# Optimization experiments

Measured on AMD Instinct MI355X. Metric: run time of the kernel, lower is better.

The kernel has to match this reference:

```python
import jax, jax.numpy as jnp
import numpy as np

H, DK = 16, 64
D = H * DK  # d_model = 1024
B, S = 2, 2048


def setup_inputs() -> dict:
    key = jax.random.key(0)
    ks = jax.random.split(key, 11)
    std = 1.0 / np.sqrt(D)
    inp = {
        "query": jax.random.normal(ks[0], (B, S, D), dtype=jnp.float32),
        "key": jax.random.normal(ks[1], (B, S, D), dtype=jnp.float32),
        "value": jax.random.normal(ks[2], (B, S, D), dtype=jnp.float32),
        "Wq": jax.random.normal(ks[3], (D, D), dtype=jnp.float32) * std,
        "bq": jnp.zeros((D,), dtype=jnp.float32),
        "Wk": jax.random.normal(ks[4], (D, D), dtype=jnp.float32) * std,
        "bk": jnp.zeros((D,), dtype=jnp.float32),
        "Wv": jax.random.normal(ks[5], (D, D), dtype=jnp.float32) * std,
        "bv": jnp.zeros((D,), dtype=jnp.float32),
        "Wo": jax.random.normal(ks[6], (D, D), dtype=jnp.float32) * std,
        "bo": jnp.zeros((D,), dtype=jnp.float32),
    }
    return inp


def reference(query, key, value, Wq, bq, Wk, bk, Wv, bv, Wo, bo):
    # torch.nn.Linear convention: y = x @ W.T + b
    def split_heads(x):
        b, s, _ = x.shape
        return x.reshape(b, s, H, DK).transpose(0, 2, 1, 3)  # [B,H,S,DK]

    q = split_heads(query @ Wq.T + bq)
    k = split_heads(key @ Wk.T + bk)
    v = split_heads(value @ Wv.T + bv)

    scale = 1.0 / jnp.sqrt(jnp.asarray(DK, dtype=q.dtype))
    scores = jnp.einsum("bhqd,bhkd->bhqk", q, k) * scale  # [B,H,S,S]
    p_attn = jax.nn.softmax(scores, axis=-1)
    ctx = jnp.einsum("bhqk,bhkd->bhqd", p_attn, v)  # [B,H,S,DK]

    ctx = ctx.transpose(0, 2, 1, 3).reshape(query.shape[0], -1, H * DK)
    return ctx @ Wo.T + bo
```

## Files before the change

### kernel.cpp

```cpp
#include <hip/hip_runtime.h>
#include <stdint.h>

#define BATCH 2
#define SEQ   2048
#define NHEAD 16
#define DK    64
#define DMODEL 1024
#define MROWS (BATCH*SEQ)

typedef __attribute__((ext_vector_type(8))) __bf16 bf16x8;
typedef __attribute__((ext_vector_type(4))) float f32x4;
typedef __attribute__((ext_vector_type(8))) unsigned short u16x8;
typedef __attribute__((ext_vector_type(4))) unsigned short u16x4;
typedef __attribute__((ext_vector_type(4))) unsigned int u32x4;

#define QSCALE 0.18033688f

__device__ __forceinline__ unsigned short f2bf(float f) {
  union { float f; uint32_t u; } c; c.f = f;
  uint32_t u = c.u;
  return (unsigned short)((u + 0x7fffu + ((u >> 16) & 1u)) >> 16);
}

__device__ __forceinline__ void gld16(const void* g, void* lds) {
  __builtin_amdgcn_global_load_lds(
      (const __attribute__((address_space(1))) void*)g,
      (__attribute__((address_space(3))) void*)lds,
      16, 0, 0);
}

__global__ __launch_bounds__(256)
void cvt_all(const float* __restrict__ q, const float* __restrict__ k, const float* __restrict__ v,
             const float* __restrict__ Wq, const float* __restrict__ Wk,
             const float* __restrict__ Wv, const float* __restrict__ Wo,
             unsigned short* __restrict__ Xq, unsigned short* __restrict__ Xk,
             unsigned short* __restrict__ Xv,
             unsigned short* __restrict__ Wqb, unsigned short* __restrict__ Wkb,
             unsigned short* __restrict__ Wvb, unsigned short* __restrict__ Wob) {
  int blk = blockIdx.x;
  const float* in; unsigned short* out; int base;
  if (blk < 6144) {
    int ti = blk >> 11;
    in  = (ti == 0) ? q  : (ti == 1) ? k  : v;
    out = (ti == 0) ? Xq : (ti == 1) ? Xk : Xv;
    base = (blk & 2047) * 2048;
  } else {
    int ti = (blk - 6144) >> 9;
    in  = (ti == 0) ? Wq  : (ti == 1) ? Wk  : (ti == 2) ? Wv  : Wo;
    out = (ti == 0) ? Wqb : (ti == 1) ? Wkb : (ti == 2) ? Wvb : Wob;
    base = ((blk - 6144) & 511) * 2048;
  }
  int i = base + threadIdx.x * 8;
  float4 a = *(const float4*)(in + i);
  float4 b = *(const float4*)(in + i + 4);
  u16x8 o;
  o[0]=f2bf(a.x); o[1]=f2bf(a.y); o[2]=f2bf(a.z); o[3]=f2bf(a.w);
  o[4]=f2bf(b.x); o[5]=f2bf(b.y); o[6]=f2bf(b.z); o[7]=f2bf(b.w);
  *(u16x8*)(out + i) = o;
}

__device__ __forceinline__ void gemm_body(const unsigned short* __restrict__ X,
                                          const unsigned short* __restrict__ W,
                                          const float* __restrict__ bias,
                                          unsigned short* __restrict__ Yb,
                                          float* __restrict__ Yf,
                                          int mode) {
  __shared__ unsigned short lA[128 * 64];
  __shared__ unsigned short lB[128 * 64];
  const int t = threadIdx.x;
  const int lane = t & 63, wave = t >> 6;
  const int cl = lane & 15, qd = lane >> 4;
  const int wm = wave >> 1, wn = wave & 1;
  const int rowBase = blockIdx.y * 128;
  const int colBase = blockIdx.x * 128;
  const int srow = t >> 3, sslot = t & 7;

  f32x4 zero = {0.f, 0.f, 0.f, 0.f};
  f32x4 acc[4][4];
  for (int mt = 0; mt < 4; mt++) for (int nt = 0; nt < 4; nt++) acc[mt][nt] = zero;

  for (int k0 = 0; k0 < DMODEL; k0 += 64) {
    __syncthreads();
    #pragma unroll
    for (int i = 0; i < 4; i++) {
      int r = i * 32 + srow;
      int chunk = sslot ^ (r & 7);
      gld16(X + (size_t)(rowBase + r) * DMODEL + k0 + chunk * 8,
            (char*)lA + i * 4096 + wave * 1024);
      gld16(W + (size_t)(colBase + r) * DMODEL + k0 + chunk * 8,
            (char*)lB + i * 4096 + wave * 1024);
    }
    __syncthreads();
    #pragma unroll
    for (int ks = 0; ks < 2; ks++) {
      bf16x8 af[4], bfr[4];
      #pragma unroll
      for (int mt = 0; mt < 4; mt++) {
        int r = wm * 64 + mt * 16 + cl;
        int slot = (ks * 4 + qd) ^ (r & 7);
        af[mt] = *(const bf16x8*)&lA[r * 64 + slot * 8];
      }
      #pragma unroll
      for (int nt = 0; nt < 4; nt++) {
        int r = wn * 64 + nt * 16 + cl;
        int slot = (ks * 4 + qd) ^ (r & 7);
        bfr[nt] = *(const bf16x8*)&lB[r * 64 + slot * 8];
      }
      #pragma unroll
      for (int mt = 0; mt < 4; mt++)
        #pragma unroll
        for (int nt = 0; nt < 4; nt++)
          acc[mt][nt] = __builtin_amdgcn_mfma_f32_16x16x32_bf16(af[mt], bfr[nt], acc[mt][nt], 0, 0, 0);
    }
  }
  if (mode == 2) {
    #pragma unroll
    for (int mt = 0; mt < 4; mt++) {
      int row0 = rowBase + wm * 64 + mt * 16 + qd * 4;
      int bb = row0 >> 11;
      int s_in = row0 & 2047;
      int blk = s_in & ~63;
      int n4 = (s_in & 63) >> 2;
      int l4 = n4 & 7;
      int pos = 8 * (n4 >> 3) + ((l4 < 4) ? 2 * l4 : 2 * (l4 - 4) + 1);
      #pragma unroll
      for (int nt = 0; nt < 4; nt++) {
        int c = colBase + wn * 64 + nt * 16 + cl;
        float bv = bias[c];
        int hh = c >> 6, d = c & 63;
        u16x4 v;
        #pragma unroll
        for (int r = 0; r < 4; r++) v[r] = f2bf(acc[mt][nt][r] + bv);
        *(u16x4*)&Yb[(size_t)((bb * NHEAD + hh) * 64 + d) * SEQ + blk + pos * 4] = v;
      }
    }
  } else {
    #pragma unroll
    for (int mt = 0; mt < 4; mt++) {
      int row = rowBase + wm * 64 + mt * 16 + qd * 4;
      #pragma unroll
      for (int nt = 0; nt < 4; nt++) {
        int c = colBase + wn * 64 + nt * 16 + cl;
        float bv = bias[c];
        #pragma unroll
        for (int r = 0; r < 4; r++) {
          float v = acc[mt][nt][r] + bv;
          if (mode == 3)      Yf[(size_t)(row + r) * DMODEL + c] = v;
          else if (mode == 1) Yb[(size_t)(row + r) * DMODEL + c] = f2bf(v * QSCALE);
          else                Yb[(size_t)(row + r) * DMODEL + c] = f2bf(v);
        }
      }
    }
  }
}

__global__ __launch_bounds__(256)
void gemm_qkv(const unsigned short* __restrict__ Xq, const unsigned short* __restrict__ Xk,
              const unsigned short* __restrict__ Xv,
              const unsigned short* __restrict__ Wq, const unsigned short* __restrict__ Wk,
              const unsigned short* __restrict__ Wv,
              const float* __restrict__ bq, const float* __restrict__ bk,
              const float* __restrict__ bv,
              unsigned short* __restrict__ Q, unsigned short* __restrict__ K,
              unsigned short* __restrict__ VT) {
  int z = blockIdx.z;
  const unsigned short* X = (z == 0) ? Xq : (z == 1) ? Xk : Xv;
  const unsigned short* W = (z == 0) ? Wq : (z == 1) ? Wk : Wv;
  const float* b = (z == 0) ? bq : (z == 1) ? bk : bv;
  unsigned short* Y = (z == 0) ? Q : (z == 1) ? K : VT;
  int mode = (z == 0) ? 1 : (z == 1) ? 0 : 2;
  gemm_body(X, W, b, Y, nullptr, mode);
}

__global__ __launch_bounds__(256)
void gemm_out(const unsigned short* __restrict__ CTX, const unsigned short* __restrict__ Wo,
              const float* __restrict__ bo, float* __restrict__ out) {
  gemm_body(CTX, Wo, bo, nullptr, out, 3);
}

__global__ __launch_bounds__(256)
void attn(const unsigned short* __restrict__ Q, const unsigned short* __restrict__ K,
          const unsigned short* __restrict__ VT, unsigned short* __restrict__ CTX) {
  __shared__ unsigned short lK[2][64 * 64];
  __shared__ unsigned short lV[2][64 * 64];
  const int t = threadIdx.x, lane = t & 63, wave = t >> 6;
  const int cl = lane & 15, qd = lane >> 4;
  const int qt = blockIdx.x, h = blockIdx.y, b = blockIdx.z;
  const int srow = t >> 3, sslot = t & 7;

  #pragma unroll
  for (int half = 0; half < 2; half++)
    #pragma unroll
    for (int i = 0; i < 2; i++) {
      int r = i * 32 + srow;
      int chunk = sslot ^ (r & 7);
      gld16(Q + (size_t)(b * SEQ + qt * 128 + half * 64 + r) * DMODEL + h * 64 + chunk * 8,
            (char*)lK[half] + i * 4096 + wave * 1024);
    }
  __syncthreads();
  bf16x8 qf[2][2];
  #pragma unroll
  for (int qg = 0; qg < 2; qg++)
    #pragma unroll
    for (int ks = 0; ks < 2; ks++) {
      int r = wave * 16 + cl;
      int slot = (ks * 4 + qd) ^ (r & 7);
      qf[qg][ks] = *(const bf16x8*)&lK[qg][r * 64 + slot * 8];
    }
  __syncthreads();

  #pragma unroll
  for (int i = 0; i < 2; i++) {
    int r = i * 32 + srow;
    int chunk = sslot ^ (r & 7);
    gld16(K + (size_t)(b * SEQ + r) * DMODEL + h * 64 + chunk * 8,
          (char*)lK[0] + i * 4096 + wave * 1024);
    gld16(VT + (size_t)((b * NHEAD + h) * 64 + r) * SEQ + chunk * 8,
          (char*)lV[0] + i * 4096 + wave * 1024);
  }

  f32x4 zero = {0.f, 0.f, 0.f, 0.f};
  f32x4 o[2][4];
  #pragma unroll
  for (int qg = 0; qg < 2; qg++)
    #pragma unroll
    for (int dt = 0; dt < 4; dt++) o[qg][dt] = zero;
  float rsum[2] = {0.f, 0.f};

  for (int kt = 0; kt < SEQ / 64; kt++) {
    const int c = kt & 1;
    __syncthreads();
    if (kt + 1 < SEQ / 64) {
      #pragma unroll
      for (int i = 0; i < 2; i++) {
        int r = i * 32 + srow;
        int chunk = sslot ^ (r & 7);
        gld16(K + (size_t)(b * SEQ + (kt + 1) * 64 + r) * DMODEL + h * 64 + chunk * 8,
              (char*)lK[c ^ 1] + i * 4096 + wave * 1024);
        gld16(VT + (size_t)((b * NHEAD + h) * 64 + r) * SEQ + (kt + 1) * 64 + chunk * 8,
              (char*)lV[c ^ 1] + i * 4096 + wave * 1024);
      }
    }

    f32x4 sc[2][4];
    #pragma unroll
    for (int qg = 0; qg < 2; qg++)
      #pragma unroll
      for (int nt = 0; nt < 4; nt++) sc[qg][nt] = zero;
    #pragma unroll
    for (int ks = 0; ks < 2; ks++)
      #pragma unroll
      for (int nt = 0; nt < 4; nt++) {
        int rk = nt * 16 + cl;
        int slot = (ks * 4 + qd) ^ (rk & 7);
        bf16x8 kf = *(const bf16x8*)&lK[c][rk * 64 + slot * 8];
        sc[0][nt] = __builtin_amdgcn_mfma_f32_16x16x32_bf16(kf, qf[0][ks], sc[0][nt], 0, 0, 0);
        sc[1][nt] = __builtin_amdgcn_mfma_f32_16x16x32_bf16(kf, qf[1][ks], sc[1][nt], 0, 0, 0);
      }

    bf16x8 pb[2][2];
    #pragma unroll
    for (int qg = 0; qg < 2; qg++)
      #pragma unroll
      for (int ntp = 0; ntp < 2; ntp++) {
        bf16x8 x;
        #pragma unroll
        for (int j = 0; j < 4; j++) {
          float v = __builtin_amdgcn_exp2f(sc[qg][2 * ntp][j]);
          rsum[qg] += v; x[j] = (__bf16)v;
        }
        #pragma unroll
        for (int j = 0; j < 4; j++) {
          float v = __builtin_amdgcn_exp2f(sc[qg][2 * ntp + 1][j]);
          rsum[qg] += v; x[4 + j] = (__bf16)v;
        }
        pb[qg][ntp] = x;
      }

    #pragma unroll
    for (int ntp = 0; ntp < 2; ntp++)
      #pragma unroll
      for (int dt = 0; dt < 4; dt++) {
        int d = dt * 16 + cl;
        int slot = (4 * ntp + qd) ^ (d & 7);
        bf16x8 vf = *(const bf16x8*)&lV[c][d * 64 + slot * 8];
        o[0][dt] = __builtin_amdgcn_mfma_f32_16x16x32_bf16(vf, pb[0][ntp], o[0][dt], 0, 0, 0);
        o[1][dt] = __builtin_amdgcn_mfma_f32_16x16x32_bf16(vf, pb[1][ntp], o[1][dt], 0, 0, 0);
      }
  }

  #pragma unroll
  for (int qg = 0; qg < 2; qg++) {
    float rs = rsum[qg];
    rs += __shfl_xor(rs, 16, 64);
    rs += __shfl_xor(rs, 32, 64);
    float inv = 1.f / rs;
    int row = b * SEQ + qt * 128 + qg * 64 + wave * 16 + cl;
    #pragma unroll
    for (int dt = 0; dt < 4; dt++) {
      u16x4 v;
      #pragma unroll
      for (int r = 0; r < 4; r++) v[r] = f2bf(o[qg][dt][r] * inv);
      *(u16x4*)&CTX[(size_t)row * DMODEL + h * 64 + dt * 16 + qd * 4] = v;
    }
  }
}

extern "C" void kernel_launch(void* const* d_in, const int* in_sizes, int n_in,
                              void* d_out, int out_size, void* d_ws, size_t ws_size,
                              hipStream_t stream) {
  const float* q  = (const float*)d_in[0];
  const float* k  = (const float*)d_in[1];
  const float* v  = (const float*)d_in[2];
  const float* Wq = (const float*)d_in[3]; const float* bq = (const float*)d_in[4];
  const float* Wk = (const float*)d_in[5]; const float* bk = (const float*)d_in[6];
  const float* Wv = (const float*)d_in[7]; const float* bv = (const float*)d_in[8];
  const float* Wo = (const float*)d_in[9]; const float* bo = (const float*)d_in[10];
  float* out = (float*)d_out;

  char* ws = (char*)d_ws;
  const size_t MB = 1u << 20;
  unsigned short* Xq  = (unsigned short*)(ws + 0 * MB);
  unsigned short* Xk  = (unsigned short*)(ws + 8 * MB);
  unsigned short* Xv  = (unsigned short*)(ws + 16 * MB);
  unsigned short* Wqb = (unsigned short*)(ws + 24 * MB);
  unsigned short* Wkb = (unsigned short*)(ws + 26 * MB);
  unsigned short* Wvb = (unsigned short*)(ws + 28 * MB);
  unsigned short* Wob = (unsigned short*)(ws + 30 * MB);
  unsigned short* Qp  = (unsigned short*)(ws + 32 * MB);
  unsigned short* Kp  = (unsigned short*)(ws + 40 * MB);
  unsigned short* VT  = (unsigned short*)(ws + 48 * MB);
  unsigned short* CTX = (unsigned short*)(ws + 56 * MB);

  cvt_all<<<8192, 256, 0, stream>>>(q, k, v, Wq, Wk, Wv, Wo,
                                    Xq, Xk, Xv, Wqb, Wkb, Wvb, Wob);

  gemm_qkv<<<dim3(DMODEL / 128, MROWS / 128, 3), 256, 0, stream>>>(
      Xq, Xk, Xv, Wqb, Wkb, Wvb, bq, bk, bv, Qp, Kp, VT);

  attn<<<dim3(SEQ / 128, NHEAD, BATCH), 256, 0, stream>>>(Qp, Kp, VT, CTX);

  gemm_out<<<dim3(DMODEL / 128, MROWS / 128), 256, 0, stream>>>(CTX, Wob, bo, out);
}
```

Measured before the change: 235.9 us.

## Split attention KV range in two and combine partials in a separate kernel

The attention kernel now splits the key/value sequence into two halves, doubling the grid. Each block writes unnormalized fp32 partial outputs and row sums, and a new combine kernel adds the halves, normalizes, and converts to bf16. This is meant to raise parallelism and CU occupancy for the attention stage. In exchange it adds a large fp32 partial buffer written and read through global memory, plus an extra kernel launch. Scratch space reuses the input-conversion area and the output buffer, and the Wo copy is moved to avoid overlap.

```diff
diff --git a/kernel.cpp b/kernel.cpp
--- a/kernel.cpp
+++ b/kernel.cpp
@@ -12,7 +12,6 @@
 typedef __attribute__((ext_vector_type(4))) float f32x4;
 typedef __attribute__((ext_vector_type(8))) unsigned short u16x8;
 typedef __attribute__((ext_vector_type(4))) unsigned short u16x4;
-typedef __attribute__((ext_vector_type(4))) unsigned int u32x4;
 
 #define QSCALE 0.18033688f
 
@@ -180,13 +179,16 @@
 
 __global__ __launch_bounds__(256)
 void attn(const unsigned short* __restrict__ Q, const unsigned short* __restrict__ K,
-          const unsigned short* __restrict__ VT, unsigned short* __restrict__ CTX) {
+          const unsigned short* __restrict__ VT,
+          float* __restrict__ Opart, float* __restrict__ Spart) {
   __shared__ unsigned short lK[2][64 * 64];
   __shared__ unsigned short lV[2][64 * 64];
   const int t = threadIdx.x, lane = t & 63, wave = t >> 6;
   const int cl = lane & 15, qd = lane >> 4;
-  const int qt = blockIdx.x, h = blockIdx.y, b = blockIdx.z;
+  const int qt = blockIdx.x, h = blockIdx.y;
+  const int b = blockIdx.z & 1, sp = blockIdx.z >> 1;
   const int srow = t >> 3, sslot = t & 7;
+  const int kt0 = sp * 16;
 
   #pragma unroll
   for (int half = 0; half < 2; half++)
@@ -213,9 +215,9 @@
   for (int i = 0; i < 2; i++) {
     int r = i * 32 + srow;
     int chunk = sslot ^ (r & 7);
-    gld16(K + (size_t)(b * SEQ + r) * DMODEL + h * 64 + chunk * 8,
+    gld16(K + (size_t)(b * SEQ + kt0 * 64 + r) * DMODEL + h * 64 + chunk * 8,
           (char*)lK[0] + i * 4096 + wave * 1024);
-    gld16(VT + (size_t)((b * NHEAD + h) * 64 + r) * SEQ + chunk * 8,
+    gld16(VT + (size_t)((b * NHEAD + h) * 64 + r) * SEQ + kt0 * 64 + chunk * 8,
           (char*)lV[0] + i * 4096 + wave * 1024);
   }
 
@@ -227,17 +229,17 @@
     for (int dt = 0; dt < 4; dt++) o[qg][dt] = zero;
   float rsum[2] = {0.f, 0.f};
 
-  for (int kt = 0; kt < SEQ / 64; kt++) {
+  for (int kt = 0; kt < 16; kt++) {
     const int c = kt & 1;
     __syncthreads();
-    if (kt + 1 < SEQ / 64) {
+    if (kt + 1 < 16) {
       #pragma unroll
       for (int i = 0; i < 2; i++) {
         int r = i * 32 + srow;
         int chunk = sslot ^ (r & 7);
-        gld16(K + (size_t)(b * SEQ + (kt + 1) * 64 + r) * DMODEL + h * 64 + chunk * 8,
+        gld16(K + (size_t)(b * SEQ + (kt0 + kt + 1) * 64 + r) * DMODEL + h * 64 + chunk * 8,
               (char*)lK[c ^ 1] + i * 4096 + wave * 1024);
-        gld16(VT + (size_t)((b * NHEAD + h) * 64 + r) * SEQ + (kt + 1) * 64 + chunk * 8,
+        gld16(VT + (size_t)((b * NHEAD + h) * 64 + r) * SEQ + (kt0 + kt + 1) * 64 + chunk * 8,
               (char*)lV[c ^ 1] + i * 4096 + wave * 1024);
       }
     }
@@ -294,16 +296,30 @@
     float rs = rsum[qg];
     rs += __shfl_xor(rs, 16, 64);
     rs += __shfl_xor(rs, 32, 64);
-    float inv = 1.f / rs;
     int row = b * SEQ + qt * 128 + qg * 64 + wave * 16 + cl;
-    #pragma unroll
-    for (int dt = 0; dt < 4; dt++) {
-      u16x4 v;
-      #pragma unroll
-      for (int r = 0; r < 4; r++) v[r] = f2bf(o[qg][dt][r] * inv);
-      *(u16x4*)&CTX[(size_t)row * DMODEL + h * 64 + dt * 16 + qd * 4] = v;
-    }
-  }
+    if (qd == 0) Spart[(size_t)(sp * NHEAD + h) * MROWS + row] = rs;
+    #pragma unroll
+    for (int dt = 0; dt < 4; dt++)
+      *(f32x4*)&Opart[((size_t)sp * MROWS + row) * DMODEL + h * 64 + dt * 16 + qd * 4] =
+          o[qg][dt];
+  }
+}
+
+__global__ __launch_bounds__(256)
+void combine(const float* __restrict__ Opart, const float* __restrict__ Spart,
+             unsigned short* __restrict__ CTX) {
+  int row = blockIdx.x;
+  int c = threadIdx.x * 4;
+  int h = c >> 6;
+  float s = Spart[(size_t)h * MROWS + row] +
+            Spart[(size_t)(NHEAD + h) * MROWS + row];
+  float inv = 1.f / s;
+  f32x4 a = *(const f32x4*)&Opart[(size_t)row * DMODEL + c];
+  f32x4 b2 = *(const f32x4*)&Opart[((size_t)MROWS + row) * DMODEL + c];
+  u16x4 v;
+  #pragma unroll
+  for (int r = 0; r < 4; r++) v[r] = f2bf((a[r] + b2[r]) * inv);
+  *(u16x4*)&CTX[(size_t)row * DMODEL + c] = v;
 }
 
 extern "C" void kernel_launch(void* const* d_in, const int* in_sizes, int n_in,
@@ -326,11 +342,13 @@
   unsigned short* Wqb = (unsigned short*)(ws + 24 * MB);
   unsigned short* Wkb = (unsigned short*)(ws + 26 * MB);
   unsigned short* Wvb = (unsigned short*)(ws + 28 * MB);
-  unsigned short* Wob = (unsigned short*)(ws + 30 * MB);
+  unsigned short* Wob = (unsigned short*)(ws + 70 * MB);
   unsigned short* Qp  = (unsigned short*)(ws + 32 * MB);
   unsigned short* Kp  = (unsigned short*)(ws + 40 * MB);
   unsigned short* VT  = (unsigned short*)(ws + 48 * MB);
   unsigned short* CTX = (unsigned short*)(ws + 56 * MB);
+  float* Opart = (float*)(ws + 0 * MB);
+  float* Spart = (float*)d_out;
 
   cvt_all<<<8192, 256, 0, stream>>>(q, k, v, Wq, Wk, Wv, Wo,
                                     Xq, Xk, Xv, Wqb, Wkb, Wvb, Wob);
@@ -338,7 +356,9 @@
   gemm_qkv<<<dim3(DMODEL / 128, MROWS / 128, 3), 256, 0, stream>>>(
       Xq, Xk, Xv, Wqb, Wkb, Wvb, bq, bk, bv, Qp, Kp, VT);
 
-  attn<<<dim3(SEQ / 128, NHEAD, BATCH), 256, 0, stream>>>(Qp, Kp, VT, CTX);
+  attn<<<dim3(SEQ / 128, NHEAD, BATCH * 2), 256, 0, stream>>>(Qp, Kp, VT, Opart, Spart);
+
+  combine<<<MROWS, 256, 0, stream>>>(Opart, Spart, CTX);
 
   gemm_out<<<dim3(DMODEL / 128, MROWS / 128), 256, 0, stream>>>(CTX, Wob, bo, out);
 }
```

Result: slower. 244.6 us (+3.7%).
